# Kernel optimization log

Hardware: AMD Instinct MI355X
Metric: run time of the kernel (lower is better)

Reference implementation:

```python
import jax, jax.numpy as jnp
import numpy as np


def setup_inputs() -> dict:
    key = jax.random.key(0)
    kq, kk, kv = jax.random.split(key, 3)
    d_head, sq, skv = 128, 8192, 8192
    q = jax.random.normal(kq, (d_head, sq), dtype=jnp.float32)
    k = jax.random.normal(kk, (d_head, skv), dtype=jnp.float32)
    v = jax.random.normal(kv, (d_head, skv), dtype=jnp.float32)
    return {"q": q, "k": k, "v": v}


def reference(q, k, v):
    # qk: (seqlen_q, seqlen_kv) -- full score matrix, no 1/sqrt(d) scaling (faithful)
    qk = jnp.einsum('dq,dk->qk', q, k)
    row_max = jnp.max(qk, axis=1, keepdims=True)
    exp_row = jnp.exp(qk - row_max)
    scores = exp_row / jnp.sum(exp_row, axis=1, keepdims=True)
    # attn_out: (seqlen_q, d_head)
    attn_out = jnp.einsum('qk,dk->qd', scores, v)
    return attn_out
```

## Files before the change

### kernel.cpp

```cpp
#include <hip/hip_runtime.h>
#include <hip/hip_bf16.h>
#include <math.h>

typedef _Float16 half8 __attribute__((ext_vector_type(8)));
typedef _Float16 half4v __attribute__((ext_vector_type(4)));
typedef __fp16 fp16x2 __attribute__((ext_vector_type(2)));
typedef float f32x4 __attribute__((ext_vector_type(4)));
typedef float f32x16 __attribute__((ext_vector_type(16)));

#define D 128
#define SQ 8192
#define SKV 8192
#define BQ 128
#define BKV 64
#define LOG2E 1.4426950408889634f
#define DEFER_THR 11.5417f

__device__ __forceinline__ ushort f2bf(float x) {
  union { float f; unsigned u; } v; v.f = x;
  unsigned r = v.u + 0x7fffu + ((v.u >> 16) & 1u);
  return (ushort)(r >> 16);
}
__device__ __forceinline__ float bf2f(ushort h) {
  union { unsigned u; float f; } v; v.u = ((unsigned)h) << 16;
  return v.f;
}
__device__ __forceinline__ unsigned cvtpk_bf(float a, float b) {
  unsigned r;
  asm("v_cvt_pk_bf16_f32 %0, %1, %2" : "=v"(r) : "v"(a), "v"(b));
  return r;
}
__device__ __forceinline__ unsigned cvtpk_h(float a, float b) {
  union { fp16x2 h; unsigned u; } r;
  r.h = __builtin_amdgcn_cvt_pkrtz(a, b);
  return r.u;
}
__device__ __forceinline__ float fexp2(float x) {
  float r;
  asm("v_exp_f32 %0, %1" : "=v"(r) : "v"(x));
  return r;
}
__device__ __forceinline__ void pl32swap(unsigned& a, unsigned& b) {
  asm("v_permlane32_swap_b32 %0, %1" : "+v"(a), "+v"(b));
}

__global__ void prep_q(const float* __restrict__ src, _Float16* __restrict__ dst) {
  __shared__ float tile[32][33];
  int s0 = blockIdx.x * 32, d0 = blockIdx.y * 32;
  int t = threadIdx.x, g = t >> 5, l = t & 31;
#pragma unroll
  for (int j = 0; j < 4; ++j)
    tile[g * 4 + j][l] = src[(size_t)(d0 + g * 4 + j) * SQ + s0 + l];
  __syncthreads();
#pragma unroll
  for (int j = 0; j < 4; ++j) {
    int sl = g * 4 + j;
    dst[(size_t)(s0 + sl) * D + d0 + l] = (_Float16)(tile[l][sl] * LOG2E);
  }
}

__global__ void prep_k(const float* __restrict__ src, _Float16* __restrict__ dst) {
  __shared__ float tile[32][33];
  int s0 = blockIdx.x * 32, d0 = blockIdx.y * 32;
  int t = threadIdx.x, g = t >> 5, l = t & 31;
#pragma unroll
  for (int j = 0; j < 4; ++j)
    tile[g * 4 + j][l] = src[(size_t)(d0 + g * 4 + j) * SKV + s0 + l];
  __syncthreads();
#pragma unroll
  for (int j = 0; j < 4; ++j) {
    int srow = s0 + g * 4 + j;
    int dcol = d0 + l;
    size_t elem = (size_t)((srow >> 5) * 8 + (dcol >> 4)) * 512 +
                  (((dcol >> 3) & 1) * 32 + (srow & 31)) * 8 + (dcol & 7);
    dst[elem] = (_Float16)tile[l][g * 4 + j];
  }
}

__global__ void prep_v(const float* __restrict__ src, _Float16* __restrict__ dst) {
  int i4 = (blockIdx.x * 256 + threadIdx.x) * 4;
  float4 v = *(const float4*)(src + i4);
  int drow = i4 >> 13;
  int kv = i4 & (SKV - 1);
  size_t elem = (size_t)(kv >> 6) * 8192 +
                (size_t)((drow >> 5) * 4 + ((kv >> 4) & 3)) * 512 +
                (((kv >> 3) & 1) * 32 + (drow & 31)) * 8 + (kv & 7);
  half4v o = { (_Float16)v.x, (_Float16)v.y, (_Float16)v.z, (_Float16)v.w };
  *(half4v*)(dst + elem) = o;
}

__global__ __launch_bounds__(256, 2)
void flash_fwd(const _Float16* __restrict__ QT, const _Float16* __restrict__ PK,
               const _Float16* __restrict__ PV,
               ushort* __restrict__ Opart, float* __restrict__ Mst,
               float* __restrict__ Lst, int splitLen) {
  __shared__ _Float16 Kl[2][BKV * D];
  __shared__ _Float16 Vl[2][BKV * D];

  const int tid = threadIdx.x;
  const int w = tid >> 6;
  const int lane = tid & 63;
  const int lc = lane & 31;
  const int hi = lane >> 5;
  const int qb = blockIdx.x;
  const int split = blockIdx.y;
  const int qrow = qb * BQ + w * 32 + lc;

  half8 qh[8];
#pragma unroll
  for (int ds = 0; ds < 8; ++ds)
    qh[ds] = *(const half8*)(QT + (size_t)qrow * D + ds * 16 + hi * 8);

  f32x16 Ot[4];
#pragma unroll
  for (int dt = 0; dt < 4; ++dt)
#pragma unroll
    for (int e = 0; e < 16; ++e) Ot[dt][e] = 0.f;
  float mrun = -INFINITY, lrun = 0.f;

  const int kvBase = split * splitLen;
  const int nsteps = splitLen / BKV;

#define STAGE(NB, KV0)                                                        \
  {                                                                           \
    _Pragma("unroll")                                                         \
    for (int j = 0; j < 8; ++j) {                                             \
      int cblk = w * 8 + j;                                                   \
      int cc = cblk & 15;                                                     \
      const _Float16* gp = ((cblk < 16) ? PK : PV) +                          \
                           (size_t)(KV0) * D + cc * 512 + lane * 8;           \
      _Float16* lp = ((cblk < 16) ? &Kl[NB][0] : &Vl[NB][0]) + cc * 512;      \
      __builtin_amdgcn_global_load_lds(                                       \
          (const __attribute__((address_space(1))) unsigned*)gp,              \
          (__attribute__((address_space(3))) unsigned*)lp, 16, 0, 0);         \
    }                                                                         \
  }

  STAGE(0, kvBase);
  __syncthreads();
  int cur = 0;

  for (int it = 0; it < nsteps; ++it) {
    const int kv0 = kvBase + it * BKV;
    const bool more = (it + 1 < nsteps);
    if (more) STAGE(cur ^ 1, kv0 + BKV);

    const _Float16* kb = &Kl[cur][0] + lane * 8;
    const _Float16* vb = &Vl[cur][0] + lane * 8;

    half8 ka[16];
#pragma unroll
    for (int j = 0; j < 16; ++j) ka[j] = *(const half8*)(kb + j * 512);

    f32x16 s0, s1;
#pragma unroll
    for (int e = 0; e < 16; ++e) { s0[e] = 0.f; s1[e] = 0.f; }
    __builtin_amdgcn_s_setprio(1);
#pragma unroll
    for (int ds = 0; ds < 8; ++ds) {
      s0 = __builtin_amdgcn_mfma_f32_32x32x16_f16(ka[ds], qh[ds], s0, 0, 0, 0);
      s1 = __builtin_amdgcn_mfma_f32_32x32x16_f16(ka[8 + ds], qh[ds], s1, 0, 0, 0);
    }
    __builtin_amdgcn_s_setprio(0);

    half8 va[16];
#pragma unroll
    for (int f = 0; f < 16; ++f) va[f] = *(const half8*)(vb + f * 512);

    float t8[8];
#pragma unroll
    for (int e = 0; e < 8; ++e)
      t8[e] = fmaxf(fmaxf(s0[e], s0[e + 8]), fmaxf(s1[e], s1[e + 8]));
    float mx = fmaxf(fmaxf(fmaxf(t8[0], t8[4]), fmaxf(t8[1], t8[5])),
                     fmaxf(fmaxf(t8[2], t8[6]), fmaxf(t8[3], t8[7])));
    mx = fmaxf(mx, __shfl_xor(mx, 32));

    if (!__all(mx - mrun <= DEFER_THR)) {
      float mn = fmaxf(mrun, mx);
      float sc = fexp2(mrun - mn);
      mrun = mn;
      lrun *= sc;
#pragma unroll
      for (int dt = 0; dt < 4; ++dt)
#pragma unroll
        for (int e = 0; e < 16; ++e) Ot[dt][e] *= sc;
    }

#pragma unroll
    for (int e = 0; e < 16; ++e) {
      s0[e] = fexp2(s0[e] - mrun);
      s1[e] = fexp2(s1[e] - mrun);
    }
    float a8[8];
#pragma unroll
    for (int e = 0; e < 8; ++e) a8[e] = (s0[e] + s0[e + 8]) + (s1[e] + s1[e + 8]);
    float lsum = ((a8[0] + a8[4]) + (a8[1] + a8[5])) +
                 ((a8[2] + a8[6]) + (a8[3] + a8[7]));
    lsum += __shfl_xor(lsum, 32);
    lrun += lsum;

    unsigned pk[8];
    half8 pb[4];
    union { unsigned u[4]; half8 v; } pbu;
#pragma unroll
    for (int j = 0; j < 8; ++j) pk[j] = cvtpk_h(s0[2 * j], s0[2 * j + 1]);
    pl32swap(pk[0], pk[2]); pl32swap(pk[1], pk[3]);
    pl32swap(pk[4], pk[6]); pl32swap(pk[5], pk[7]);
    pbu.u[0] = pk[0]; pbu.u[1] = pk[1]; pbu.u[2] = pk[2]; pbu.u[3] = pk[3]; pb[0] = pbu.v;
    pbu.u[0] = pk[4]; pbu.u[1] = pk[5]; pbu.u[2] = pk[6]; pbu.u[3] = pk[7]; pb[1] = pbu.v;
#pragma unroll
    for (int j = 0; j < 8; ++j) pk[j] = cvtpk_h(s1[2 * j], s1[2 * j + 1]);
    pl32swap(pk[0], pk[2]); pl32swap(pk[1], pk[3]);
    pl32swap(pk[4], pk[6]); pl32swap(pk[5], pk[7]);
    pbu.u[0] = pk[0]; pbu.u[1] = pk[1]; pbu.u[2] = pk[2]; pbu.u[3] = pk[3]; pb[2] = pbu.v;
    pbu.u[0] = pk[4]; pbu.u[1] = pk[5]; pbu.u[2] = pk[6]; pbu.u[3] = pk[7]; pb[3] = pbu.v;

    __builtin_amdgcn_s_setprio(1);
#pragma unroll
    for (int cc = 0; cc < 4; ++cc) {
      Ot[0] = __builtin_amdgcn_mfma_f32_32x32x16_f16(va[0 * 4 + cc], pb[cc], Ot[0], 0, 0, 0);
      Ot[1] = __builtin_amdgcn_mfma_f32_32x32x16_f16(va[1 * 4 + cc], pb[cc], Ot[1], 0, 0, 0);
      Ot[2] = __builtin_amdgcn_mfma_f32_32x32x16_f16(va[2 * 4 + cc], pb[cc], Ot[2], 0, 0, 0);
      Ot[3] = __builtin_amdgcn_mfma_f32_32x32x16_f16(va[3 * 4 + cc], pb[cc], Ot[3], 0, 0, 0);
    }
    __builtin_amdgcn_s_setprio(0);

    __syncthreads();
    cur ^= 1;
  }

  ushort* Op = Opart + (size_t)split * SQ * D + (size_t)qrow * D;
#pragma unroll
  for (int dt = 0; dt < 4; ++dt) {
#pragma unroll
    for (int rg = 0; rg < 4; ++rg) {
      uint2 o2;
      o2.x = cvtpk_bf(Ot[dt][4 * rg + 0], Ot[dt][4 * rg + 1]);
      o2.y = cvtpk_bf(Ot[dt][4 * rg + 2], Ot[dt][4 * rg + 3]);
      *(uint2*)(Op + dt * 32 + rg * 8 + hi * 4) = o2;
    }
  }
  if (hi == 0) {
    Mst[split * SQ + qrow] = mrun;
    Lst[split * SQ + qrow] = lrun;
  }
}

__global__ void combine(const ushort* __restrict__ Opart, const float* __restrict__ Mst,
                        const float* __restrict__ Lst, float* __restrict__ out, int nsplit) {
  int t4 = (blockIdx.x * 256 + threadIdx.x) * 4;
  int qi = t4 >> 7;
  float M = -INFINITY;
  for (int s = 0; s < nsplit; ++s) M = fmaxf(M, Mst[s * SQ + qi]);
  float n0 = 0.f, n1 = 0.f, n2 = 0.f, n3 = 0.f, den = 0.f;
  for (int s = 0; s < nsplit; ++s) {
    float wgt = fexp2(Mst[s * SQ + qi] - M);
    den += wgt * Lst[s * SQ + qi];
    ushort4 u = *(const ushort4*)(Opart + (size_t)s * SQ * D + t4);
    n0 += wgt * bf2f(u.x); n1 += wgt * bf2f(u.y);
    n2 += wgt * bf2f(u.z); n3 += wgt * bf2f(u.w);
  }
  float inv = 1.0f / den;
  float4 o = { n0 * inv, n1 * inv, n2 * inv, n3 * inv };
  *(float4*)(out + t4) = o;
}

extern "C" void kernel_launch(void* const* d_in, const int* in_sizes, int n_in,
                              void* d_out, int out_size, void* d_ws, size_t ws_size,
                              hipStream_t stream) {
  const float* q = (const float*)d_in[0];
  const float* k = (const float*)d_in[1];
  const float* v = (const float*)d_in[2];
  float* out = (float*)d_out;

  char* ws = (char*)d_ws;
  const size_t mat = (size_t)SQ * D * 2;
  _Float16* QT = (_Float16*)(ws);
  _Float16* PK = (_Float16*)(ws + mat);
  _Float16* PV = (_Float16*)(ws + 2 * mat);
  char* rest = ws + 3 * mat;

  const size_t opartSz = (size_t)SQ * D * 2;
  const size_t statSz  = (size_t)SQ * 4;
  int nsplit = 8;
  while (nsplit > 1 &&
         3 * mat + (size_t)nsplit * (opartSz + 2 * statSz) > ws_size) nsplit >>= 1;

  ushort* Opart = (ushort*)rest;
  float* Mst = (float*)(rest + (size_t)nsplit * opartSz);
  float* Lst = (float*)(rest + (size_t)nsplit * opartSz + (size_t)nsplit * statSz);

  prep_q<<<dim3(SQ / 32, D / 32), 256, 0, stream>>>(q, QT);
  prep_k<<<dim3(SKV / 32, D / 32), 256, 0, stream>>>(k, PK);
  prep_v<<<(D * SKV) / (256 * 4), 256, 0, stream>>>(v, PV);
  flash_fwd<<<dim3(SQ / BQ, nsplit), 256, 0, stream>>>(QT, PK, PV,
                                                       Opart, Mst, Lst, SKV / nsplit);
  combine<<<(SQ * D) / (256 * 4), 256, 0, stream>>>(Opart, Mst, Lst, out, nsplit);
}
```

Measured before the change: 65.45 us.

## Fuse Q/K/V prep kernels into one launch and stagger half the split blocks

Merges the three layout-conversion kernels into a single prep_all launch. Q and K tiles now cover all 128 head dims per block and are written as 16-byte half8 vectors, and V is converted 8 elements per thread. This cuts launch overhead and widens the stores. Separately, flash_fwd blocks with blockIdx.y bit 4 set now sleep briefly at start, apparently to stagger memory traffic between split groups. That sleep adds latency and its benefit is speculative.

Measured after the change: 60.31 us. -7.9%, faster.

```diff
diff --git a/kernel.cpp b/kernel.cpp
--- a/kernel.cpp
+++ b/kernel.cpp
@@ -3,7 +3,6 @@
 #include <math.h>
 
 typedef _Float16 half8 __attribute__((ext_vector_type(8)));
-typedef _Float16 half4v __attribute__((ext_vector_type(4)));
 typedef __fp16 fp16x2 __attribute__((ext_vector_type(2)));
 typedef float f32x4 __attribute__((ext_vector_type(4)));
 typedef float f32x16 __attribute__((ext_vector_type(16)));
@@ -44,49 +43,55 @@
   asm("v_permlane32_swap_b32 %0, %1" : "+v"(a), "+v"(b));
 }
 
-__global__ void prep_q(const float* __restrict__ src, _Float16* __restrict__ dst) {
-  __shared__ float tile[32][33];
-  int s0 = blockIdx.x * 32, d0 = blockIdx.y * 32;
-  int t = threadIdx.x, g = t >> 5, l = t & 31;
-#pragma unroll
-  for (int j = 0; j < 4; ++j)
-    tile[g * 4 + j][l] = src[(size_t)(d0 + g * 4 + j) * SQ + s0 + l];
-  __syncthreads();
-#pragma unroll
-  for (int j = 0; j < 4; ++j) {
-    int sl = g * 4 + j;
-    dst[(size_t)(s0 + sl) * D + d0 + l] = (_Float16)(tile[l][sl] * LOG2E);
-  }
-}
-
-__global__ void prep_k(const float* __restrict__ src, _Float16* __restrict__ dst) {
-  __shared__ float tile[32][33];
-  int s0 = blockIdx.x * 32, d0 = blockIdx.y * 32;
-  int t = threadIdx.x, g = t >> 5, l = t & 31;
-#pragma unroll
-  for (int j = 0; j < 4; ++j)
-    tile[g * 4 + j][l] = src[(size_t)(d0 + g * 4 + j) * SKV + s0 + l];
-  __syncthreads();
-#pragma unroll
-  for (int j = 0; j < 4; ++j) {
-    int srow = s0 + g * 4 + j;
-    int dcol = d0 + l;
-    size_t elem = (size_t)((srow >> 5) * 8 + (dcol >> 4)) * 512 +
-                  (((dcol >> 3) & 1) * 32 + (srow & 31)) * 8 + (dcol & 7);
-    dst[elem] = (_Float16)tile[l][g * 4 + j];
-  }
-}
-
-__global__ void prep_v(const float* __restrict__ src, _Float16* __restrict__ dst) {
-  int i4 = (blockIdx.x * 256 + threadIdx.x) * 4;
-  float4 v = *(const float4*)(src + i4);
-  int drow = i4 >> 13;
-  int kv = i4 & (SKV - 1);
-  size_t elem = (size_t)(kv >> 6) * 8192 +
-                (size_t)((drow >> 5) * 4 + ((kv >> 4) & 3)) * 512 +
-                (((kv >> 3) & 1) * 32 + (drow & 31)) * 8 + (kv & 7);
-  half4v o = { (_Float16)v.x, (_Float16)v.y, (_Float16)v.z, (_Float16)v.w };
-  *(half4v*)(dst + elem) = o;
+__global__ void prep_all(const float* __restrict__ q, const float* __restrict__ k,
+                         const float* __restrict__ v,
+                         _Float16* __restrict__ QT, _Float16* __restrict__ PK,
+                         _Float16* __restrict__ PV) {
+  int b = blockIdx.x;
+  int t = threadIdx.x;
+  if (b < 512) {
+    const bool isQ = (b < 256);
+    const float* src = isQ ? q : k;
+    const float scl = isQ ? LOG2E : 1.0f;
+    int s0 = (isQ ? b : b - 256) * 32;
+    __shared__ float lds[128][33];
+    int dr = t >> 5, l = t & 31;
+#pragma unroll
+    for (int j = 0; j < 16; ++j) {
+      int dd = dr * 16 + j;
+      lds[dd][l] = src[(size_t)dd * SQ + s0 + l];
+    }
+    __syncthreads();
+#pragma unroll
+    for (int i = 0; i < 2; ++i) {
+      int cid = t + i * 256;
+      int c = cid >> 5, sl = cid & 31;
+      half8 hv;
+#pragma unroll
+      for (int e = 0; e < 8; ++e) hv[e] = (_Float16)(lds[c * 8 + e][sl] * scl);
+      if (isQ) {
+        *(half8*)(QT + (size_t)(s0 + sl) * D + c * 8) = hv;
+      } else {
+        int srow = s0 + sl;
+        size_t elem = (size_t)((srow >> 5) * 8 + (c >> 1)) * 512 +
+                      ((c & 1) * 32 + (srow & 31)) * 8;
+        *(half8*)(PK + elem) = hv;
+      }
+    }
+  } else {
+    int idx = (b - 512) * 256 + t;
+    int i8 = idx * 8;
+    float4 x0 = *(const float4*)(v + i8);
+    float4 x1 = *(const float4*)(v + i8 + 4);
+    int drow = i8 >> 13;
+    int kv = i8 & (SKV - 1);
+    size_t elem = (size_t)(kv >> 6) * 8192 +
+                  (size_t)((drow >> 5) * 4 + ((kv >> 4) & 3)) * 512 +
+                  (((kv >> 3) & 1) * 32 + (drow & 31)) * 8;
+    half8 hv = { (_Float16)x0.x, (_Float16)x0.y, (_Float16)x0.z, (_Float16)x0.w,
+                 (_Float16)x1.x, (_Float16)x1.y, (_Float16)x1.z, (_Float16)x1.w };
+    *(half8*)(PV + elem) = hv;
+  }
 }
 
 __global__ __launch_bounds__(256, 2)
@@ -96,6 +101,8 @@
                float* __restrict__ Lst, int splitLen) {
   __shared__ _Float16 Kl[2][BKV * D];
   __shared__ _Float16 Vl[2][BKV * D];
+
+  if (blockIdx.y & 4) __builtin_amdgcn_s_sleep(60);
 
   const int tid = threadIdx.x;
   const int w = tid >> 6;
@@ -290,9 +297,7 @@
   float* Mst = (float*)(rest + (size_t)nsplit * opartSz);
   float* Lst = (float*)(rest + (size_t)nsplit * opartSz + (size_t)nsplit * statSz);
 
-  prep_q<<<dim3(SQ / 32, D / 32), 256, 0, stream>>>(q, QT);
-  prep_k<<<dim3(SKV / 32, D / 32), 256, 0, stream>>>(k, PK);
-  prep_v<<<(D * SKV) / (256 * 4), 256, 0, stream>>>(v, PV);
+  prep_all<<<1024, 256, 0, stream>>>(q, k, v, QT, PK, PV);
   flash_fwd<<<dim3(SQ / BQ, nsplit), 256, 0, stream>>>(QT, PK, PV,
                                                        Opart, Mst, Lst, SKV / nsplit);
   combine<<<(SQ * D) / (256 * 4), 256, 0, stream>>>(Opart, Mst, Lst, out, nsplit);
```
